# Performance work log

Measured on AMD Instinct MI355X. Metric: run time of the kernel, lower is better.

The kernel has to match this reference:

```python
import jax, jax.numpy as jnp
import numpy as np

NH = 8          # n_heads
CLIP = 10.0     # tanh_clipping


def _make_heads(x):
    # (B, n, H) -> (B, NH, n, H//NH)
    B, n, H = x.shape
    return x.reshape(B, n, NH, H // NH).transpose(0, 2, 1, 3)


def setup_inputs() -> dict:
    key = jax.random.key(0)
    ks = jax.random.split(key, 12)
    B, N, G, H = 64, 2000, 128, 128
    s = 1.0 / np.sqrt(H)
    embeddings = jax.random.normal(ks[0], (B, N, H), jnp.float32)
    u = jax.random.uniform(ks[1], (B, G, N))
    group_ninf_mask = jnp.where(u < 0.1, -1e9, 0.0).astype(jnp.float32)
    w = lambda k: (jax.random.normal(k, (H, H), jnp.float32) * s)
    return {
        'embeddings': embeddings,
        'group_ninf_mask': group_ninf_mask,
        'Wq_graph': w(ks[2]), 'Wq_source': w(ks[3]), 'Wq_target': w(ks[4]),
        'Wq_last': w(ks[5]), 'Wk': w(ks[6]), 'Wv': w(ks[7]),
        'Wc': w(ks[8]), 'bc': jnp.zeros((H,), jnp.float32),
        'source_node': jax.random.randint(ks[9], (B,), 0, N),
        'target_node': jax.random.randint(ks[10], (B,), 0, N),
        'last_node': jax.random.randint(ks[11], (B, G), 0, N),
    }


def reference(embeddings, group_ninf_mask, Wq_graph, Wq_source, Wq_target,
              Wq_last, Wk, Wv, Wc, bc, source_node, target_node, last_node):
    B, N, H = embeddings.shape
    G = group_ninf_mask.shape[1]
    hd = H // NH
    b = jnp.arange(B)

    # --- reset() state ---
    graph_emb = embeddings.mean(axis=1, keepdims=True)              # (B,1,H)
    q_graph = _make_heads(graph_emb @ Wq_graph.T)                   # (B,NH,1,hd)
    src_emb = embeddings[b, source_node][:, None, :]                # (B,1,H)
    q_source = _make_heads(src_emb @ Wq_source.T)
    tgt_emb = embeddings[b, target_node][:, None, :]                # (B,1,H)
    q_target = _make_heads(tgt_emb @ Wq_target.T)
    glimpse_k = _make_heads(embeddings @ Wk.T)                      # (B,NH,N,hd)
    glimpse_v = _make_heads(embeddings @ Wv.T)                      # (B,NH,N,hd)

    # --- forward(last_node) ---
    last_emb = embeddings[b[:, None], last_node]                    # (B,G,H)
    q_last = _make_heads(last_emb @ Wq_last.T)                      # (B,NH,G,hd)
    glimpse_q = q_graph + q_source + q_target + q_last              # (B,NH,G,hd)

    scores = jnp.einsum('bhgd,bhnd->bhgn', glimpse_q, glimpse_k) / np.sqrt(hd)
    scores = scores + group_ninf_mask[:, None, :, :]                # mask per head
    attn = jax.nn.softmax(scores, axis=-1)                          # (B,NH,G,N)
    heads = jnp.einsum('bhgn,bhnd->bhgd', attn, glimpse_v)          # (B,NH,G,hd)
    mh_out = heads.transpose(0, 2, 1, 3).reshape(B, G, H)           # (B,G,H)
    final_q = mh_out @ Wc.T + bc                                    # multi_head_combine

    # single-head logits vs logit_k = embeddings^T, tanh-clipped + masked
    logits = jnp.einsum('bgh,bnh->bgn', final_q, embeddings) / np.sqrt(H)
    logits = CLIP * jnp.tanh(logits) + group_ninf_mask
    probs = jax.nn.softmax(logits, axis=2)                          # (B,G,N)
    return probs
```

## Files before the change

kernel.cpp:

```cpp
#include <hip/hip_runtime.h>
#include <hip/hip_bf16.h>

#define BB 64
#define NN 2000
#define GG 128
#define HH 128
#define NHEAD 8
#define HD 16

typedef __attribute__((ext_vector_type(8))) short short8;
typedef __attribute__((ext_vector_type(4))) float f32x4;

__device__ __forceinline__ unsigned short bf16hi(float f) {
    union { float f; unsigned u; } v; v.f = f;
    return (unsigned short)(v.u >> 16);
}
__device__ __forceinline__ float bf16tof(unsigned short h) {
    union { float f; unsigned u; } v; v.u = ((unsigned)h) << 16;
    return v.f;
}

__device__ __forceinline__ void cvt8(const float4& v0, const float4& v1,
                                     short8& hi, short8& lo) {
    float fv[8] = {v0.x, v0.y, v0.z, v0.w, v1.x, v1.y, v1.z, v1.w};
#pragma unroll
    for (int i = 0; i < 8; ++i) {
        unsigned short h = bf16hi(fv[i]);
        hi[i] = (short)h;
        lo[i] = (short)bf16hi(fv[i] - bf16tof(h));
    }
}

__device__ __forceinline__ void fma8x8(const float4& a0, const float4& a1,
                                       const float4& b0, const float4& b1,
                                       float acc[8][8]) {
    const float av[8] = {a0.x, a0.y, a0.z, a0.w, a1.x, a1.y, a1.z, a1.w};
    const float bv[8] = {b0.x, b0.y, b0.z, b0.w, b1.x, b1.y, b1.z, b1.w};
#pragma unroll
    for (int i = 0; i < 8; ++i)
#pragma unroll
        for (int k = 0; k < 8; ++k) acc[i][k] += av[i] * bv[k];
}

__global__ __launch_bounds__(256) void k_wt(const float* w0, const float* w1, const float* w2,
                     const float* w3, const float* w4, const float* w5,
                     const float* w6, float* WT,
                     unsigned short* Wkhi, unsigned short* Wklo,
                     unsigned short* Wvhi, unsigned short* Wvlo) {
    int m = blockIdx.x;
    if (m >= 5) {
        const float* src = (m == 5) ? w4 : w5;
        unsigned short* dh = (m == 5) ? Wkhi : Wvhi;
        unsigned short* dl = (m == 5) ? Wklo : Wvlo;
        for (int e = threadIdx.x * 4; e < 16384; e += 1024) {
            float4 v = *(const float4*)(src + e);
            float fv[4] = {v.x, v.y, v.z, v.w};
            unsigned short h4[4], l4[4];
#pragma unroll
            for (int i = 0; i < 4; ++i) {
                h4[i] = bf16hi(fv[i]); l4[i] = bf16hi(fv[i] - bf16tof(h4[i]));
            }
            uint2 ph, pl;
            ph.x = h4[0] | (h4[1] << 16); ph.y = h4[2] | (h4[3] << 16);
            pl.x = l4[0] | (l4[1] << 16); pl.y = l4[2] | (l4[3] << 16);
            *(uint2*)(dh + e) = ph;
            *(uint2*)(dl + e) = pl;
        }
        return;
    }
    __shared__ float t[128 * 129];
    const float* src = (m == 0) ? w0 : (m == 1) ? w1 : (m == 2) ? w2 : (m == 3) ? w3 : w6;
    int slot = (m == 4) ? 6 : m;
    for (int e = threadIdx.x; e < 16384; e += 256) {
        int c = e >> 7, j = e & 127;
        t[c * 129 + j] = src[e];
    }
    __syncthreads();
    for (int e = threadIdx.x; e < 16384; e += 256) {
        int j = e >> 7, c = e & 127;
        WT[slot * 16384 + e] = t[c * 129 + j];
    }
}

__global__ __launch_bounds__(256) void k_maskbits(const float* mask, unsigned long long* bits) {
    int bg = blockIdx.x;
    int lane = threadIdx.x & 63;
    int wv = threadIdx.x >> 6;
    for (int w = wv; w < 32; w += 4) {
        int n = w * 64 + lane;
        bool keep = false;
        if (n < NN) keep = (mask[(size_t)bg * NN + n] == 0.0f);
        unsigned long long bal = __ballot(keep);
        if (lane == 0) bits[bg * 32 + w] = bal;
    }
}

__global__ __launch_bounds__(128) void k_gsum(const float* emb, float* gpart) {
    int ck = blockIdx.x, b = blockIdx.y, c = threadIdx.x;
    const float* p = emb + ((size_t)b * NN + ck * 125) * HH + c;
    float s = 0.0f;
#pragma unroll 5
    for (int r = 0; r < 125; ++r) s += p[(size_t)r * HH];
    gpart[ck * 8192 + b * 128 + c] = s;
}

__global__ __launch_bounds__(128) void k_qbase(const float* emb, const int* srcn, const int* tgtn,
                        const float* gpart, const float* WT, float* qbase) {
    int b = blockIdx.x, c = threadIdx.x;
    __shared__ float ge[128], se[128], te[128];
    float s = 0.0f;
#pragma unroll
    for (int t = 0; t < 16; ++t) s += gpart[t * 8192 + b * 128 + c];
    ge[c] = s * (1.0f / 2000.0f);
    se[c] = emb[((size_t)b * NN + srcn[b]) * HH + c];
    te[c] = emb[((size_t)b * NN + tgtn[b]) * HH + c];
    __syncthreads();
    const float* Wg = WT;
    const float* Ws = WT + 16384;
    const float* Wt2 = WT + 32768;
    float acc = 0.0f;
#pragma unroll 4
    for (int j = 0; j < 128; ++j) {
        acc += ge[j] * Wg[j * 128 + c] + se[j] * Ws[j * 128 + c] + te[j] * Wt2[j * 128 + c];
    }
    qbase[b * 128 + c] = acc;
}

__global__ __launch_bounds__(256) void k_qlast(const float* emb, const int* lastn, const float* WT,
                        const float* qbase, unsigned short* Qhi, unsigned short* Qlo) {
    int b = blockIdx.x;
    int tid = threadIdx.x, xq = tid & 15, yq = tid >> 4;
    __shared__ float Bl[128 * 132];
    for (int e = tid; e < 16384; e += 256) {
        int g = e >> 7, j = e & 127;
        Bl[j * 132 + g] = emb[((size_t)b * NN + lastn[b * 128 + g]) * HH + j];
    }
    __syncthreads();
    const float* Wql = WT + 3 * 16384;
    float acc[8][8] = {};
#pragma unroll 4
    for (int j = 0; j < 128; ++j) {
        const float4* Ar = (const float4*)(Wql + j * 128);
        float4 a0 = Ar[yq], a1 = Ar[16 + yq];
        const float4* Br = (const float4*)(Bl + j * 132);
        float4 b0 = Br[xq], b1 = Br[16 + xq];
        fma8x8(a0, a1, b0, b1, acc);
    }
    float4 qb0 = *(const float4*)(qbase + b * 128 + 4 * yq);
    float4 qb1 = *(const float4*)(qbase + b * 128 + 64 + 4 * yq);
    const float q0v[4] = {qb0.x, qb0.y, qb0.z, qb0.w};
    const float q1v[4] = {qb1.x, qb1.y, qb1.z, qb1.w};
#pragma unroll
    for (int k = 0; k < 8; ++k) {
        int g = (k < 4) ? (4 * xq + k) : (64 + 4 * xq + (k - 4));
        size_t base = ((size_t)b * 128 + g) * 128;
        unsigned short h4[4], l4[4];
#pragma unroll
        for (int i = 0; i < 4; ++i) {
            float f = (acc[i][k] + q0v[i]) * 0.25f;
            h4[i] = bf16hi(f); l4[i] = bf16hi(f - bf16tof(h4[i]));
        }
        uint2 ph, pl;
        ph.x = h4[0] | (h4[1] << 16); ph.y = h4[2] | (h4[3] << 16);
        pl.x = l4[0] | (l4[1] << 16); pl.y = l4[2] | (l4[3] << 16);
        *(uint2*)(Qhi + base + 4 * yq) = ph;
        *(uint2*)(Qlo + base + 4 * yq) = pl;
#pragma unroll
        for (int i = 0; i < 4; ++i) {
            float f = (acc[4 + i][k] + q1v[i]) * 0.25f;
            h4[i] = bf16hi(f); l4[i] = bf16hi(f - bf16tof(h4[i]));
        }
        ph.x = h4[0] | (h4[1] << 16); ph.y = h4[2] | (h4[3] << 16);
        pl.x = l4[0] | (l4[1] << 16); pl.y = l4[2] | (l4[3] << 16);
        *(uint2*)(Qhi + base + 64 + 4 * yq) = ph;
        *(uint2*)(Qlo + base + 64 + 4 * yq) = pl;
    }
}

__global__ __launch_bounds__(256, 4) void k_kv(const float* emb,
        const unsigned short* Wkhi, const unsigned short* Wklo,
        const unsigned short* Wvhi, const unsigned short* Wvlo,
        unsigned short* Khi, unsigned short* Klo,
        unsigned short* Vhi, unsigned short* Vlo) {
    int nt = blockIdx.x, b = blockIdx.y;
    int tid = threadIdx.x;
    int wv = tid >> 6, lane = tid & 63, l15 = lane & 15, q3 = lane >> 4;
    int n0 = nt * 128;

    short8 eh[2][4], el[2][4];
#pragma unroll
    for (int t = 0; t < 2; ++t) {
        int n = n0 + wv * 32 + t * 16 + l15;
        const float* rowp = emb + ((size_t)b * NN + n) * HH + q3 * 8;
        bool ok = (n < NN);
#pragma unroll
        for (int ks = 0; ks < 4; ++ks) {
            float4 v0 = make_float4(0.f, 0.f, 0.f, 0.f), v1 = v0;
            if (ok) {
                v0 = *(const float4*)(rowp + ks * 32);
                v1 = *(const float4*)(rowp + ks * 32 + 4);
            }
            cvt8(v0, v1, eh[t][ks], el[t][ks]);
        }
    }

#pragma unroll
    for (int ct = 0; ct < 8; ++ct) {
        f32x4 aK[2] = {{0.f, 0.f, 0.f, 0.f}, {0.f, 0.f, 0.f, 0.f}};
        f32x4 aV[2] = {{0.f, 0.f, 0.f, 0.f}, {0.f, 0.f, 0.f, 0.f}};
#pragma unroll
        for (int ks = 0; ks < 4; ++ks) {
            size_t woff = ((size_t)(ct * 16 + l15)) * 128 + ks * 32 + q3 * 8;
            short8 wkh = *(const short8*)(Wkhi + woff);
            short8 wkl = *(const short8*)(Wklo + woff);
            short8 wvh = *(const short8*)(Wvhi + woff);
            short8 wvl = *(const short8*)(Wvlo + woff);
#pragma unroll
            for (int t = 0; t < 2; ++t) {
                aK[t] = __builtin_amdgcn_mfma_f32_16x16x32_bf16(wkh, eh[t][ks], aK[t], 0, 0, 0);
                aK[t] = __builtin_amdgcn_mfma_f32_16x16x32_bf16(wkh, el[t][ks], aK[t], 0, 0, 0);
                aK[t] = __builtin_amdgcn_mfma_f32_16x16x32_bf16(wkl, eh[t][ks], aK[t], 0, 0, 0);
                aV[t] = __builtin_amdgcn_mfma_f32_16x16x32_bf16(eh[t][ks], wvh, aV[t], 0, 0, 0);
                aV[t] = __builtin_amdgcn_mfma_f32_16x16x32_bf16(el[t][ks], wvh, aV[t], 0, 0, 0);
                aV[t] = __builtin_amdgcn_mfma_f32_16x16x32_bf16(eh[t][ks], wvl, aV[t], 0, 0, 0);
            }
        }
#pragma unroll
        for (int t = 0; t < 2; ++t) {
            int kn = n0 + wv * 32 + t * 16 + l15;
            if (kn < NN) {
                unsigned short h4[4], l4[4];
#pragma unroll
                for (int r = 0; r < 4; ++r) {
                    float f = aK[t][r];
                    h4[r] = bf16hi(f); l4[r] = bf16hi(f - bf16tof(h4[r]));
                }
                uint2 ph, pl;
                ph.x = h4[0] | (h4[1] << 16); ph.y = h4[2] | (h4[3] << 16);
                pl.x = l4[0] | (l4[1] << 16); pl.y = l4[2] | (l4[3] << 16);
                size_t kbase = (((size_t)b * 8 + ct) * 2000 + kn) * 16 + 4 * q3;
                *(uint2*)(Khi + kbase) = ph;
                *(uint2*)(Klo + kbase) = pl;
            }
            int nb = n0 + wv * 32 + t * 16 + 4 * q3;
            if (nb + 3 < NN) {
                unsigned short h4[4], l4[4];
#pragma unroll
                for (int r = 0; r < 4; ++r) {
                    float f = aV[t][r];
                    h4[r] = bf16hi(f); l4[r] = bf16hi(f - bf16tof(h4[r]));
                }
                uint2 ph, pl;
                ph.x = h4[0] | (h4[1] << 16); ph.y = h4[2] | (h4[3] << 16);
                pl.x = l4[0] | (l4[1] << 16); pl.y = l4[2] | (l4[3] << 16);
                size_t vbase = (((size_t)b * 8 + ct) * 16 + l15) * 2000 + nb;
                *(uint2*)(Vhi + vbase) = ph;
                *(uint2*)(Vlo + vbase) = pl;
            }
        }
    }
}

__global__ __launch_bounds__(256) void k_flash(const unsigned short* Khi, const unsigned short* Klo,
                        const unsigned short* Vhi, const unsigned short* Vlo,
                        const unsigned short* Qhi, const unsigned short* Qlo,
                        const unsigned long long* bits, float* Opart, float* Zpart) {
    int bid = blockIdx.x;
    int s4 = bid & 3, h = (bid >> 2) & 7, b = bid >> 5;
    int tid = threadIdx.x;
    int wv = tid >> 6, lane = tid & 63, l15 = lane & 15, q3 = lane >> 4;

    __shared__ unsigned short Klds[2][64][24];
    __shared__ unsigned short Vlds[2][16][72];
    __shared__ unsigned short Plds[4][2][32][72];

    const short8 z8 = {0, 0, 0, 0, 0, 0, 0, 0};

    short8 qf[2][2];
#pragma unroll
    for (int gt = 0; gt < 2; ++gt) {
        int g = wv * 32 + gt * 16 + l15;
        if (q3 < 2) {
            size_t off = ((size_t)b * 128 + g) * 128 + h * 16 + q3 * 8;
            qf[gt][0] = *(const short8*)(Qhi + off);
            qf[gt][1] = *(const short8*)(Qlo + off);
        } else {
            qf[gt][0] = z8; qf[gt][1] = z8;
        }
    }

    f32x4 Oacc[2] = {{0.f, 0.f, 0.f, 0.f}, {0.f, 0.f, 0.f, 0.f}};
    float zacc[2] = {0.f, 0.f};

    const unsigned long long* bb0 = bits + (((size_t)b * 128 + wv * 32 + l15) * 32);
    const unsigned long long* bb1 = bb0 + 16 * 32;

    size_t kvbase = ((size_t)b * 8 + h);
    const unsigned short* Kh = Khi + kvbase * 2000 * 16;
    const unsigned short* Kl = Klo + kvbase * 2000 * 16;
    const unsigned short* Vh = Vhi + kvbase * 16 * 2000;
    const unsigned short* Vl = Vlo + kvbase * 16 * 2000;

    int snr = tid >> 2, sj4 = (tid & 3) * 4;
    int svd = tid >> 4, svn = (tid & 15) * 4;

    for (int ch = s4 * 8; ch < s4 * 8 + 8; ++ch) {
        int n0 = ch * 64;
        __syncthreads();
        {
            uint2 zz; zz.x = 0; zz.y = 0;
            int n = n0 + snr;
            uint2 k0 = zz, k1 = zz;
            if (n < NN) {
                size_t off = ((size_t)n) * 16 + sj4;
                k0 = *(const uint2*)(Kh + off);
                k1 = *(const uint2*)(Kl + off);
            }
            *(uint2*)&Klds[0][snr][sj4] = k0;
            *(uint2*)&Klds[1][snr][sj4] = k1;
            int vn = n0 + svn;
            uint2 v0 = zz, v1 = zz;
            if (vn + 3 < NN) {
                size_t off = ((size_t)svd) * 2000 + vn;
                v0 = *(const uint2*)(Vh + off);
                v1 = *(const uint2*)(Vl + off);
            }
            *(uint2*)&Vlds[0][svd][svn] = v0;
            *(uint2*)&Vlds[1][svd][svn] = v1;
        }
        __syncthreads();

        unsigned long long wm0 = bb0[ch];
        unsigned long long wm1 = bb1[ch];

        f32x4 S[4][2];
#pragma unroll
        for (int nt = 0; nt < 4; ++nt) {
            short8 kh, kl;
            if (q3 < 2) {
                kh = *(const short8*)&Klds[0][nt * 16 + l15][q3 * 8];
                kl = *(const short8*)&Klds[1][nt * 16 + l15][q3 * 8];
            } else { kh = z8; kl = z8; }
#pragma unroll
            for (int gt = 0; gt < 2; ++gt) {
                f32x4 c = {0.f, 0.f, 0.f, 0.f};
                c = __builtin_amdgcn_mfma_f32_16x16x32_bf16(kh, qf[gt][0], c, 0, 0, 0);
                c = __builtin_amdgcn_mfma_f32_16x16x32_bf16(kh, qf[gt][1], c, 0, 0, 0);
                c = __builtin_amdgcn_mfma_f32_16x16x32_bf16(kl, qf[gt][0], c, 0, 0, 0);
                S[nt][gt] = c;
            }
        }

#pragma unroll
        for (int nt = 0; nt < 4; ++nt) {
#pragma unroll
            for (int gt = 0; gt < 2; ++gt) {
                unsigned long long wm = gt ? wm1 : wm0;
                float p[4];
#pragma unroll
                for (int r = 0; r < 4; ++r) {
                    int sh = nt * 16 + q3 * 4 + r;
                    float e = ((wm >> sh) & 1ull) ? __expf(S[nt][gt][r]) : 0.0f;
                    p[r] = e;
                    zacc[gt] += e;
                }
                unsigned short h4[4], l4[4];
#pragma unroll
                for (int r = 0; r < 4; ++r) {
                    h4[r] = bf16hi(p[r]); l4[r] = bf16hi(p[r] - bf16tof(h4[r]));
                }
                uint2 ph, pl;
                ph.x = h4[0] | (h4[1] << 16); ph.y = h4[2] | (h4[3] << 16);
                pl.x = l4[0] | (l4[1] << 16); pl.y = l4[2] | (l4[3] << 16);
                *(uint2*)&Plds[wv][0][gt * 16 + l15][nt * 16 + q3 * 4] = ph;
                *(uint2*)&Plds[wv][1][gt * 16 + l15][nt * 16 + q3 * 4] = pl;
            }
        }

#pragma unroll
        for (int ks = 0; ks < 2; ++ks) {
            short8 vh = *(const short8*)&Vlds[0][l15][ks * 32 + q3 * 8];
            short8 vl = *(const short8*)&Vlds[1][l15][ks * 32 + q3 * 8];
#pragma unroll
            for (int gt = 0; gt < 2; ++gt) {
                short8 ph = *(const short8*)&Plds[wv][0][gt * 16 + l15][ks * 32 + q3 * 8];
                short8 pl = *(const short8*)&Plds[wv][1][gt * 16 + l15][ks * 32 + q3 * 8];
                Oacc[gt] = __builtin_amdgcn_mfma_f32_16x16x32_bf16(vh, ph, Oacc[gt], 0, 0, 0);
                Oacc[gt] = __builtin_amdgcn_mfma_f32_16x16x32_bf16(vh, pl, Oacc[gt], 0, 0, 0);
                Oacc[gt] = __builtin_amdgcn_mfma_f32_16x16x32_bf16(vl, ph, Oacc[gt], 0, 0, 0);
            }
        }
    }

    size_t obase = (((size_t)s4 * 64 + b) * 8 + h);
#pragma unroll
    for (int gt = 0; gt < 2; ++gt) {
        float z = zacc[gt];
        z += __shfl_xor(z, 16);
        z += __shfl_xor(z, 32);
        int g = wv * 32 + gt * 16 + l15;
        if (q3 == 0) Zpart[obase * 128 + g] = z;
#pragma unroll
        for (int r = 0; r < 4; ++r) {
            int d = q3 * 4 + r;
            Opart[(obase * 16 + d) * 128 + g] = Oacc[gt][r];
        }
    }
}

__global__ __launch_bounds__(256) void k_ocomb(const float* Opart, const float* Zpart, float* MHt) {
    int bh = blockIdx.x;
    int b = bh >> 3, h = bh & 7;
    int tid = threadIdx.x;
    for (int e = tid; e < 2048; e += 256) {
        int d = e >> 7, g = e & 127;
        float z = 0.0f, o = 0.0f;
#pragma unroll
        for (int s = 0; s < 4; ++s) {
            z += Zpart[(((size_t)s * 64 + b) * 8 + h) * 128 + g];
            o += Opart[((((size_t)s * 64 + b) * 8 + h) * 16 + d) * 128 + g];
        }
        MHt[((size_t)b * 128 + h * 16 + d) * 128 + g] = o / z;
    }
}

__global__ __launch_bounds__(256) void k_fq(const float* MHt, const float* WT, const float* bcv,
                                            unsigned short* FQhi, unsigned short* FQlo) {
    int b = blockIdx.x;
    int tid = threadIdx.x, xq = tid & 15, yq = tid >> 4;
    __shared__ float Bl[128 * 132];
    for (int e = tid; e < 16384; e += 256) {
        int j = e >> 7, g = e & 127;
        Bl[j * 132 + g] = MHt[(size_t)b * 16384 + e];
    }
    __syncthreads();
    const float* Wc = WT + 6 * 16384;
    float acc[8][8] = {};
#pragma unroll 4
    for (int j = 0; j < 128; ++j) {
        const float4* Ar = (const float4*)(Wc + j * 128);
        float4 a0 = Ar[yq], a1 = Ar[16 + yq];
        const float4* Br = (const float4*)(Bl + j * 132);
        float4 b0 = Br[xq], b1 = Br[16 + xq];
        fma8x8(a0, a1, b0, b1, acc);
    }
    float4 bc0 = *(const float4*)(bcv + 4 * yq);
    float4 bc1 = *(const float4*)(bcv + 64 + 4 * yq);
    const float bcv8[8] = {bc0.x, bc0.y, bc0.z, bc0.w, bc1.x, bc1.y, bc1.z, bc1.w};
    const float sc = 0.08838834764831845f;
#pragma unroll
    for (int k = 0; k < 8; ++k) {
        int g = (k < 4) ? (4 * xq + k) : (64 + 4 * xq + (k - 4));
        size_t base = ((size_t)b * 128 + g) * 128;
        unsigned short h4[4], l4[4];
#pragma unroll
        for (int i = 0; i < 4; ++i) {
            float f = (acc[i][k] + bcv8[i]) * sc;
            h4[i] = bf16hi(f); l4[i] = bf16hi(f - bf16tof(h4[i]));
        }
        uint2 ph, pl;
        ph.x = h4[0] | (h4[1] << 16); ph.y = h4[2] | (h4[3] << 16);
        pl.x = l4[0] | (l4[1] << 16); pl.y = l4[2] | (l4[3] << 16);
        *(uint2*)(FQhi + base + 4 * yq) = ph;
        *(uint2*)(FQlo + base + 4 * yq) = pl;
#pragma unroll
        for (int i = 0; i < 4; ++i) {
            float f = (acc[4 + i][k] + bcv8[4 + i]) * sc;
            h4[i] = bf16hi(f); l4[i] = bf16hi(f - bf16tof(h4[i]));
        }
        ph.x = h4[0] | (h4[1] << 16); ph.y = h4[2] | (h4[3] << 16);
        pl.x = l4[0] | (l4[1] << 16); pl.y = l4[2] | (l4[3] << 16);
        *(uint2*)(FQhi + base + 64 + 4 * yq) = ph;
        *(uint2*)(FQlo + base + 64 + 4 * yq) = pl;
    }
}

__global__ __launch_bounds__(256, 4) void k_logits(const float* emb,
        const unsigned short* FQhi, const unsigned short* FQlo,
        const unsigned long long* bits, float* out, float* Zp) {
    int nt = blockIdx.x, b = blockIdx.y;
    int tid = threadIdx.x;
    int wv = tid >> 6, lane = tid & 63, l15 = lane & 15, q3 = lane >> 4;
    int n0 = nt * 128;

    short8 beh[2][4], bel[2][4];
#pragma unroll
    for (int t = 0; t < 2; ++t) {
        int n = n0 + wv * 32 + t * 16 + l15;
        const float* rowp = emb + ((size_t)b * NN + n) * HH + q3 * 8;
        bool ok = (n < NN);
#pragma unroll
        for (int ks = 0; ks < 4; ++ks) {
            float4 v0 = make_float4(0.f, 0.f, 0.f, 0.f), v1 = v0;
            if (ok) {
                v0 = *(const float4*)(rowp + ks * 32);
                v1 = *(const float4*)(rowp + ks * 32 + 4);
            }
            cvt8(v0, v1, beh[t][ks], bel[t][ks]);
        }
    }

    const unsigned long long* bb = bits + (size_t)b * 128 * 32;
    int g = 0;
#pragma unroll
    for (int gt = 0; gt < 8; ++gt) {
        f32x4 acc[2] = {{0.f, 0.f, 0.f, 0.f}, {0.f, 0.f, 0.f, 0.f}};
#pragma unroll
        for (int ks = 0; ks < 4; ++ks) {
            size_t foff = ((size_t)b * 128 + gt * 16 + l15) * 128 + ks * 32 + q3 * 8;
            short8 fh = *(const short8*)(FQhi + foff);
            short8 fl = *(const short8*)(FQlo + foff);
#pragma unroll
            for (int t = 0; t < 2; ++t) {
                acc[t] = __builtin_amdgcn_mfma_f32_16x16x32_bf16(beh[t][ks], fh, acc[t], 0, 0, 0);
                acc[t] = __builtin_amdgcn_mfma_f32_16x16x32_bf16(bel[t][ks], fh, acc[t], 0, 0, 0);
                acc[t] = __builtin_amdgcn_mfma_f32_16x16x32_bf16(beh[t][ks], fl, acc[t], 0, 0, 0);
            }
        }
        g = gt * 16 + l15;
        float psum = 0.f;
#pragma unroll
        for (int t = 0; t < 2; ++t) {
            int nb = n0 + wv * 32 + t * 16 + 4 * q3;
            int word = (n0 + wv * 32 + t * 16) >> 6;
            unsigned long long wm = bb[g * 32 + word];
            float pv[4];
#pragma unroll
            for (int r = 0; r < 4; ++r) {
                int n = nb + r;
                float l = acc[t][r];
                float e2 = __expf(2.0f * l);
                float th = 1.0f - 2.0f / (e2 + 1.0f);
                float p = ((wm >> (n & 63)) & 1ull) ? __expf(10.0f * th) : 0.0f;
                pv[r] = p;
                psum += p;
            }
            if (nb + 3 < NN) {
                *(float4*)(out + ((size_t)b * 128 + g) * NN + nb) =
                    make_float4(pv[0], pv[1], pv[2], pv[3]);
            }
        }
        psum += __shfl_xor(psum, 16);
        psum += __shfl_xor(psum, 32);
        if (q3 == 0) Zp[((size_t)(nt * 4 + wv)) * 8192 + b * 128 + g] = psum;
    }
}

__global__ __launch_bounds__(256) void k_norm(const float* Zp, float* out) {
    int bg = blockIdx.x;
    __shared__ float invs;
    if (threadIdx.x == 0) {
        float s = 0.0f;
#pragma unroll
        for (int t = 0; t < 64; ++t) s += Zp[(size_t)t * 8192 + bg];
        invs = 1.0f / s;
    }
    __syncthreads();
    float inv = invs;
    for (int n = threadIdx.x; n < NN; n += 256) out[(size_t)bg * NN + n] *= inv;
}

extern "C" void kernel_launch(void* const* d_in, const int* in_sizes, int n_in,
                              void* d_out, int out_size, void* d_ws, size_t ws_size,
                              hipStream_t stream) {
    const float* emb = (const float*)d_in[0];
    const float* mask = (const float*)d_in[1];
    const float* Wqg = (const float*)d_in[2];
    const float* Wqs = (const float*)d_in[3];
    const float* Wqt = (const float*)d_in[4];
    const float* Wql = (const float*)d_in[5];
    const float* Wk = (const float*)d_in[6];
    const float* Wv = (const float*)d_in[7];
    const float* Wc = (const float*)d_in[8];
    const float* bc = (const float*)d_in[9];
    const int* srcn = (const int*)d_in[10];
    const int* tgtn = (const int*)d_in[11];
    const int* lastn = (const int*)d_in[12];
    float* out = (float*)d_out;

    float* ws = (float*)d_ws;
    float* WT = ws;
    unsigned short* Wkhi = (unsigned short*)(WT + 4 * 16384);
    unsigned short* Wklo = Wkhi + 16384;
    unsigned short* Wvhi = Wklo + 16384;
    unsigned short* Wvlo = Wvhi + 16384;
    float* gpart = ws + 114688;
    float* qbase = ws + 245760;
    float* MHt = ws + 253952;
    unsigned short* FQhi = (unsigned short*)(ws + 1302528);
    unsigned short* FQlo = FQhi + 1048576;
    float* Zp = ws + 2351104;
    unsigned short* Khi = (unsigned short*)(ws + 3399680);
    unsigned short* Klo = (unsigned short*)(ws + 11591680);
    unsigned short* Vhi = (unsigned short*)(ws + 19783680);
    unsigned short* Vlo = (unsigned short*)(ws + 27975680);
    unsigned long long* bits = (unsigned long long*)(ws + 36167680);

    float* Opart = out;
    float* Zpart = out + 4194304;
    unsigned short* Qhi = (unsigned short*)(out + 4456448);
    unsigned short* Qlo = Qhi + 1048576;

    k_wt<<<7, 256, 0, stream>>>(Wqg, Wqs, Wqt, Wql, Wk, Wv, Wc, WT, Wkhi, Wklo, Wvhi, Wvlo);
    k_maskbits<<<8192, 256, 0, stream>>>(mask, bits);
    k_gsum<<<dim3(16, 64), 128, 0, stream>>>(emb, gpart);
    k_kv<<<dim3(16, 64), 256, 0, stream>>>(emb, Wkhi, Wklo, Wvhi, Wvlo, Khi, Klo, Vhi, Vlo);
    k_qbase<<<64, 128, 0, stream>>>(emb, srcn, tgtn, gpart, WT, qbase);
    k_qlast<<<64, 256, 0, stream>>>(emb, lastn, WT, qbase, Qhi, Qlo);
    k_flash<<<2048, 256, 0, stream>>>(Khi, Klo, Vhi, Vlo, Qhi, Qlo, bits, Opart, Zpart);
    k_ocomb<<<512, 256, 0, stream>>>(Opart, Zpart, MHt);
    k_fq<<<64, 256, 0, stream>>>(MHt, WT, bc, FQhi, FQlo);
    k_logits<<<dim3(16, 64), 256, 0, stream>>>(emb, FQhi, FQlo, bits, out, Zp);
    k_norm<<<8192, 256, 0, stream>>>(Zp, out);
}
```

Baseline: 361.0 us.

## Fuse output combine into fq, use exp2 with log2e-folded Q scale, cheaper tanh

Removes the separate k_ocomb launch by folding the partial O/Z reduction and normalization into k_fq's shared-memory staging, eliminating the MHt round trip. Folds log2(e) into the Q scale so the flash kernel can use the hardware exp2 instruction instead of __expf. Replaces the division in the tanh-clipped logits with a fast reciprocal. Parallelizes the k_norm partial-sum reduction across a wavefront with shuffles instead of a single-thread serial loop. The fast reciprocal and exp2 change rounding slightly.

```diff
diff --git a/kernel.cpp b/kernel.cpp
--- a/kernel.cpp
+++ b/kernel.cpp
@@ -146,6 +146,7 @@
         float4 b0 = Br[xq], b1 = Br[16 + xq];
         fma8x8(a0, a1, b0, b1, acc);
     }
+    const float QSC = 0.36067376022224085f;
     float4 qb0 = *(const float4*)(qbase + b * 128 + 4 * yq);
     float4 qb1 = *(const float4*)(qbase + b * 128 + 64 + 4 * yq);
     const float q0v[4] = {qb0.x, qb0.y, qb0.z, qb0.w};
@@ -157,7 +158,7 @@
         unsigned short h4[4], l4[4];
 #pragma unroll
         for (int i = 0; i < 4; ++i) {
-            float f = (acc[i][k] + q0v[i]) * 0.25f;
+            float f = (acc[i][k] + q0v[i]) * QSC;
             h4[i] = bf16hi(f); l4[i] = bf16hi(f - bf16tof(h4[i]));
         }
         uint2 ph, pl;
@@ -167,7 +168,7 @@
         *(uint2*)(Qlo + base + 4 * yq) = pl;
 #pragma unroll
         for (int i = 0; i < 4; ++i) {
-            float f = (acc[4 + i][k] + q1v[i]) * 0.25f;
+            float f = (acc[4 + i][k] + q1v[i]) * QSC;
             h4[i] = bf16hi(f); l4[i] = bf16hi(f - bf16tof(h4[i]));
         }
         ph.x = h4[0] | (h4[1] << 16); ph.y = h4[2] | (h4[3] << 16);
@@ -296,10 +297,10 @@
     const unsigned long long* bb1 = bb0 + 16 * 32;
 
     size_t kvbase = ((size_t)b * 8 + h);
-    const unsigned short* Kh = Khi + kvbase * 2000 * 16;
-    const unsigned short* Kl = Klo + kvbase * 2000 * 16;
-    const unsigned short* Vh = Vhi + kvbase * 16 * 2000;
-    const unsigned short* Vl = Vlo + kvbase * 16 * 2000;
+    const unsigned short* Kh = Khi + kvbase * 32000;
+    const unsigned short* Kl = Klo + kvbase * 32000;
+    const unsigned short* Vh = Vhi + kvbase * 32000;
+    const unsigned short* Vl = Vlo + kvbase * 32000;
 
     int snr = tid >> 2, sj4 = (tid & 3) * 4;
     int svd = tid >> 4, svn = (tid & 15) * 4;
@@ -360,7 +361,7 @@
 #pragma unroll
                 for (int r = 0; r < 4; ++r) {
                     int sh = nt * 16 + q3 * 4 + r;
-                    float e = ((wm >> sh) & 1ull) ? __expf(S[nt][gt][r]) : 0.0f;
+                    float e = ((wm >> sh) & 1ull) ? __builtin_amdgcn_exp2f(S[nt][gt][r]) : 0.0f;
                     p[r] = e;
                     zacc[gt] += e;
                 }
@@ -408,30 +409,30 @@
     }
 }
 
-__global__ __launch_bounds__(256) void k_ocomb(const float* Opart, const float* Zpart, float* MHt) {
-    int bh = blockIdx.x;
-    int b = bh >> 3, h = bh & 7;
-    int tid = threadIdx.x;
-    for (int e = tid; e < 2048; e += 256) {
-        int d = e >> 7, g = e & 127;
-        float z = 0.0f, o = 0.0f;
-#pragma unroll
-        for (int s = 0; s < 4; ++s) {
-            z += Zpart[(((size_t)s * 64 + b) * 8 + h) * 128 + g];
-            o += Opart[((((size_t)s * 64 + b) * 8 + h) * 16 + d) * 128 + g];
-        }
-        MHt[((size_t)b * 128 + h * 16 + d) * 128 + g] = o / z;
-    }
-}
-
-__global__ __launch_bounds__(256) void k_fq(const float* MHt, const float* WT, const float* bcv,
+__global__ __launch_bounds__(256) void k_fq(const float* Opart, const float* Zpart,
+                                            const float* WT, const float* bcv,
                                             unsigned short* FQhi, unsigned short* FQlo) {
     int b = blockIdx.x;
     int tid = threadIdx.x, xq = tid & 15, yq = tid >> 4;
     __shared__ float Bl[128 * 132];
+    __shared__ float zinv[8][128];
+    for (int e = tid; e < 1024; e += 256) {
+        int h = e >> 7, g = e & 127;
+        float z = 0.0f;
+#pragma unroll
+        for (int s = 0; s < 4; ++s)
+            z += Zpart[(((size_t)s * 64 + b) * 8 + h) * 128 + g];
+        zinv[h][g] = 1.0f / z;
+    }
+    __syncthreads();
     for (int e = tid; e < 16384; e += 256) {
         int j = e >> 7, g = e & 127;
-        Bl[j * 132 + g] = MHt[(size_t)b * 16384 + e];
+        int h = j >> 4, d = j & 15;
+        float o = 0.0f;
+#pragma unroll
+        for (int s = 0; s < 4; ++s)
+            o += Opart[((((size_t)s * 64 + b) * 8 + h) * 16 + d) * 128 + g];
+        Bl[j * 132 + g] = o * zinv[h][g];
     }
     __syncthreads();
     const float* Wc = WT + 6 * 16384;
@@ -530,8 +531,8 @@
                 int n = nb + r;
                 float l = acc[t][r];
                 float e2 = __expf(2.0f * l);
-                float th = 1.0f - 2.0f / (e2 + 1.0f);
-                float p = ((wm >> (n & 63)) & 1ull) ? __expf(10.0f * th) : 0.0f;
+                float th10 = 10.0f - 20.0f * __builtin_amdgcn_rcpf(e2 + 1.0f);
+                float p = ((wm >> (n & 63)) & 1ull) ? __expf(th10) : 0.0f;
                 pv[r] = p;
                 psum += p;
             }
@@ -549,15 +550,16 @@
 __global__ __launch_bounds__(256) void k_norm(const float* Zp, float* out) {
     int bg = blockIdx.x;
     __shared__ float invs;
-    if (threadIdx.x == 0) {
-        float s = 0.0f;
-#pragma unroll
-        for (int t = 0; t < 64; ++t) s += Zp[(size_t)t * 8192 + bg];
-        invs = 1.0f / s;
+    int tid = threadIdx.x;
+    if (tid < 64) {
+        float s = Zp[(size_t)tid * 8192 + bg];
+#pragma unroll
+        for (int m = 1; m <= 32; m <<= 1) s += __shfl_xor(s, m);
+        if (tid == 0) invs = 1.0f / s;
     }
     __syncthreads();
     float inv = invs;
-    for (int n = threadIdx.x; n < NN; n += 256) out[(size_t)bg * NN + n] *= inv;
+    for (int n = tid; n < NN; n += 256) out[(size_t)bg * NN + n] *= inv;
 }
 
 extern "C" void kernel_launch(void* const* d_in, const int* in_sizes, int n_in,
@@ -586,7 +588,6 @@
     unsigned short* Wvlo = Wvhi + 16384;
     float* gpart = ws + 114688;
     float* qbase = ws + 245760;
-    float* MHt = ws + 253952;
     unsigned short* FQhi = (unsigned short*)(ws + 1302528);
     unsigned short* FQlo = FQhi + 1048576;
     float* Zp = ws + 2351104;
@@ -608,8 +609,7 @@
     k_qbase<<<64, 128, 0, stream>>>(emb, srcn, tgtn, gpart, WT, qbase);
     k_qlast<<<64, 256, 0, stream>>>(emb, lastn, WT, qbase, Qhi, Qlo);
     k_flash<<<2048, 256, 0, stream>>>(Khi, Klo, Vhi, Vlo, Qhi, Qlo, bits, Opart, Zpart);
-    k_ocomb<<<512, 256, 0, stream>>>(Opart, Zpart, MHt);
-    k_fq<<<64, 256, 0, stream>>>(MHt, WT, bc, FQhi, FQlo);
+    k_fq<<<64, 256, 0, stream>>>(Opart, Zpart, WT, bc, FQhi, FQlo);
     k_logits<<<dim3(16, 64), 256, 0, stream>>>(emb, FQhi, FQlo, bits, out, Zp);
     k_norm<<<8192, 256, 0, stream>>>(Zp, out);
 }
```

After: 347.4 us. 1.04x faster.
